# Kernel tuning notes

Hardware: AMD Instinct MI355X
Metric: run time of the kernel (lower is better)

The kernel has to match this reference:

```python
import jax, jax.numpy as jnp
import numpy as np

B, T, C = 1, 2_000_000, 16
NAN_FRAC = 0.05  # fraction of entries replaced by NaN, as the layer is a NaN-interpolation op


def setup_inputs() -> dict:
    key = jax.random.key(0)
    k_x, k_m = jax.random.split(key)
    x = jax.random.normal(k_x, (B, T, C), dtype=jnp.float32)
    nan_mask = jax.random.uniform(k_m, (B, T, C)) < NAN_FRAC
    x = jnp.where(nan_mask, jnp.float32(jnp.nan), x)
    return {"inputs": x}


def reference(inputs):
    # Vectorized form of the per-column loop: for each column, compute the
    # mean of the valid (non-NaN) entries along time and fill NaNs with it.
    # (Original code computes this per column with tf.reduce_mean + tf.map_fn
    # + tf.where/tf.fill; here it is a single fused pass.)
    mask = jnp.isnan(inputs)                       # [B, T, C]
    safe = jnp.where(mask, jnp.float32(0.0), inputs)
    valid = jnp.sum(jnp.logical_not(mask).astype(inputs.dtype), axis=1)  # [B, C]
    mean = jnp.sum(safe, axis=1) / jnp.maximum(valid, 1.0)               # [B, C]
    out = jnp.where(mask, mean[:, None, :], safe)  # broadcast NaN fill
    return out
```

## Files before the change

kernel.cpp:

```cpp
#include <hip/hip_runtime.h>

#define C_COLS 16

__global__ __launch_bounds__(256) void k_reduce(const float4* __restrict__ x4,
                                                long long n4,
                                                float* __restrict__ partials) {
    const int tid = threadIdx.x;
    const long long gid = (long long)blockIdx.x * blockDim.x + tid;
    const long long stride = (long long)gridDim.x * blockDim.x;

    float s0 = 0.f, s1 = 0.f, s2 = 0.f, s3 = 0.f;
    float c0 = 0.f, c1 = 0.f, c2 = 0.f, c3 = 0.f;

    for (long long i = gid; i < n4; i += stride) {
        float4 v = x4[i];
        bool m0 = (v.x == v.x); s0 += m0 ? v.x : 0.f; c0 += m0 ? 1.f : 0.f;
        bool m1 = (v.y == v.y); s1 += m1 ? v.y : 0.f; c1 += m1 ? 1.f : 0.f;
        bool m2 = (v.z == v.z); s2 += m2 ? v.z : 0.f; c2 += m2 ? 1.f : 0.f;
        bool m3 = (v.w == v.w); s3 += m3 ? v.w : 0.f; c3 += m3 ? 1.f : 0.f;
    }

    for (int off = 4; off < 64; off <<= 1) {
        s0 += __shfl_xor(s0, off, 64);
        s1 += __shfl_xor(s1, off, 64);
        s2 += __shfl_xor(s2, off, 64);
        s3 += __shfl_xor(s3, off, 64);
        c0 += __shfl_xor(c0, off, 64);
        c1 += __shfl_xor(c1, off, 64);
        c2 += __shfl_xor(c2, off, 64);
        c3 += __shfl_xor(c3, off, 64);
    }

    __shared__ float bsum[C_COLS];
    __shared__ float bcnt[C_COLS];
    if (tid < C_COLS) { bsum[tid] = 0.f; bcnt[tid] = 0.f; }
    __syncthreads();

    if ((tid & 63) < 4) {
        const int cb = (tid & 3) * 4;
        atomicAdd(&bsum[cb + 0], s0);
        atomicAdd(&bsum[cb + 1], s1);
        atomicAdd(&bsum[cb + 2], s2);
        atomicAdd(&bsum[cb + 3], s3);
        atomicAdd(&bcnt[cb + 0], c0);
        atomicAdd(&bcnt[cb + 1], c1);
        atomicAdd(&bcnt[cb + 2], c2);
        atomicAdd(&bcnt[cb + 3], c3);
    }
    __syncthreads();

    if (tid < C_COLS) {
        partials[(long long)blockIdx.x * 32 + tid] = bsum[tid];
        partials[(long long)blockIdx.x * 32 + 16 + tid] = bcnt[tid];
    }
}

__global__ __launch_bounds__(256) void k_final(const float* __restrict__ partials,
                                               int nb,
                                               const float* __restrict__ x,
                                               long long n4, long long n,
                                               float* __restrict__ mean_out) {
    const int tid = threadIdx.x;
    const int c = tid & 15;
    const int r0 = tid >> 4;

    float s = 0.f, cnt = 0.f;
    for (int p = r0; p < nb; p += 16) {
        s   += partials[(long long)p * 32 + c];
        cnt += partials[(long long)p * 32 + 16 + c];
    }

    __shared__ float ssum[256];
    __shared__ float scnt[256];
    ssum[tid] = s;
    scnt[tid] = cnt;
    __syncthreads();

    if (tid < 16) {
        float S = 0.f, Cn = 0.f;
        for (int r = 0; r < 16; ++r) {
            S  += ssum[r * 16 + tid];
            Cn += scnt[r * 16 + tid];
        }
        for (long long j = n4 * 4; j < n; ++j) {
            if ((int)(j % 16) == tid) {
                float v = x[j];
                if (v == v) { S += v; Cn += 1.f; }
            }
        }
        mean_out[tid] = S / fmaxf(Cn, 1.f);
    }
}

__global__ __launch_bounds__(256) void k_fill(const float4* __restrict__ x4,
                                              float4* __restrict__ o4,
                                              long long n4, long long n,
                                              const float* __restrict__ mean) {
    const int tid = threadIdx.x;
    const long long gid = (long long)blockIdx.x * blockDim.x + tid;
    const long long stride = (long long)gridDim.x * blockDim.x;

    const int cb = (int)(gid & 3) * 4;
    const float m0 = mean[cb + 0];
    const float m1 = mean[cb + 1];
    const float m2 = mean[cb + 2];
    const float m3 = mean[cb + 3];

    for (long long i = gid; i < n4; i += stride) {
        float4 v = x4[i];
        v.x = (v.x == v.x) ? v.x : m0;
        v.y = (v.y == v.y) ? v.y : m1;
        v.z = (v.z == v.z) ? v.z : m2;
        v.w = (v.w == v.w) ? v.w : m3;
        o4[i] = v;
    }

    if (blockIdx.x == 0 && tid == 0) {
        const float* x = (const float*)x4;
        float* o = (float*)o4;
        for (long long j = n4 * 4; j < n; ++j) {
            float v = x[j];
            o[j] = (v == v) ? v : mean[(int)(j % 16)];
        }
    }
}

extern "C" void kernel_launch(void* const* d_in, const int* in_sizes, int n_in,
                              void* d_out, int out_size, void* d_ws, size_t ws_size,
                              hipStream_t stream) {
    const float* x = (const float*)d_in[0];
    float* out = (float*)d_out;
    const long long n = (long long)in_sizes[0];
    const long long n4 = n / 4;

    int nb1 = 1024;
    {
        long long cap = ((long long)(ws_size / 4) - 16) / 32;
        if (cap < 1) cap = 1;
        if (nb1 > cap) nb1 = (int)cap;
    }
    float* partials = (float*)d_ws;
    float* mean = partials + (long long)nb1 * 32;

    k_reduce<<<nb1, 256, 0, stream>>>((const float4*)x, n4, partials);
    k_final<<<1, 256, 0, stream>>>(partials, nb1, x, n4, n, mean);

    const int nb3 = 2048;
    k_fill<<<nb3, 256, 0, stream>>>((const float4*)x, (float4*)out, n4, n, mean);
}
```

Baseline: 252.1 us.

## Fuse reduce, finalize and fill into one cooperative kernel with grid syncs

Replaces the three launches (reduce, single-block finalize, fill) with one cooperative kernel. Two grid-wide barriers separate the partial reduction, the block-0 mean computation and the fill pass. This removes two kernel launch gaps and may let the second read of the input hit in cache, since each thread re-reads the same float4 indices it reduced. It also adds unroll pragmas and nontemporal stores for the output. The risks are that grid.sync adds its own overhead, cooperative launch limits the grid to co-resident blocks (1024x256 with launch bounds of 4 blocks per CU), and the fill pass now uses 1024 blocks instead of 2048.

```diff
diff --git a/kernel.cpp b/kernel.cpp
--- a/kernel.cpp
+++ b/kernel.cpp
@@ -1,17 +1,26 @@
 #include <hip/hip_runtime.h>
+#include <hip/hip_cooperative_groups.h>
+
+namespace cg = cooperative_groups;
 
 #define C_COLS 16
+#define NT 256
+#define NB 1024
 
-__global__ __launch_bounds__(256) void k_reduce(const float4* __restrict__ x4,
-                                                long long n4,
-                                                float* __restrict__ partials) {
+typedef float floatx4 __attribute__((ext_vector_type(4)));
+
+__global__ __launch_bounds__(NT, 4) void k_fused(const float4* __restrict__ x4,
+                                                 float4* __restrict__ o4,
+                                                 long long n4, long long n,
+                                                 float* __restrict__ ws) {
     const int tid = threadIdx.x;
-    const long long gid = (long long)blockIdx.x * blockDim.x + tid;
-    const long long stride = (long long)gridDim.x * blockDim.x;
+    const long long gid = (long long)blockIdx.x * NT + tid;
+    const long long stride = (long long)gridDim.x * NT;
 
     float s0 = 0.f, s1 = 0.f, s2 = 0.f, s3 = 0.f;
     float c0 = 0.f, c1 = 0.f, c2 = 0.f, c3 = 0.f;
 
+    #pragma unroll 4
     for (long long i = gid; i < n4; i += stride) {
         float4 v = x4[i];
         bool m0 = (v.x == v.x); s0 += m0 ? v.x : 0.f; c0 += m0 ? 1.f : 0.f;
@@ -37,68 +46,59 @@
     __syncthreads();
 
     if ((tid & 63) < 4) {
-        const int cb = (tid & 3) * 4;
-        atomicAdd(&bsum[cb + 0], s0);
-        atomicAdd(&bsum[cb + 1], s1);
-        atomicAdd(&bsum[cb + 2], s2);
-        atomicAdd(&bsum[cb + 3], s3);
-        atomicAdd(&bcnt[cb + 0], c0);
-        atomicAdd(&bcnt[cb + 1], c1);
-        atomicAdd(&bcnt[cb + 2], c2);
-        atomicAdd(&bcnt[cb + 3], c3);
+        const int cb4 = (tid & 3) * 4;
+        atomicAdd(&bsum[cb4 + 0], s0);
+        atomicAdd(&bsum[cb4 + 1], s1);
+        atomicAdd(&bsum[cb4 + 2], s2);
+        atomicAdd(&bsum[cb4 + 3], s3);
+        atomicAdd(&bcnt[cb4 + 0], c0);
+        atomicAdd(&bcnt[cb4 + 1], c1);
+        atomicAdd(&bcnt[cb4 + 2], c2);
+        atomicAdd(&bcnt[cb4 + 3], c3);
     }
     __syncthreads();
 
     if (tid < C_COLS) {
-        partials[(long long)blockIdx.x * 32 + tid] = bsum[tid];
-        partials[(long long)blockIdx.x * 32 + 16 + tid] = bcnt[tid];
+        ws[(long long)blockIdx.x * 32 + tid] = bsum[tid];
+        ws[(long long)blockIdx.x * 32 + C_COLS + tid] = bcnt[tid];
     }
-}
+    __threadfence();
 
-__global__ __launch_bounds__(256) void k_final(const float* __restrict__ partials,
-                                               int nb,
-                                               const float* __restrict__ x,
-                                               long long n4, long long n,
-                                               float* __restrict__ mean_out) {
-    const int tid = threadIdx.x;
-    const int c = tid & 15;
-    const int r0 = tid >> 4;
+    cg::this_grid().sync();
 
-    float s = 0.f, cnt = 0.f;
-    for (int p = r0; p < nb; p += 16) {
-        s   += partials[(long long)p * 32 + c];
-        cnt += partials[(long long)p * 32 + 16 + c];
+    float* mean = ws + (long long)gridDim.x * 32;
+    if (blockIdx.x == 0) {
+        const int c = tid & 15;
+        const int r0 = tid >> 4;
+        float S = 0.f, Cn = 0.f;
+        for (int p = r0; p < (int)gridDim.x; p += 16) {
+            S  += ws[(long long)p * 32 + c];
+            Cn += ws[(long long)p * 32 + 16 + c];
+        }
+        __shared__ float ssum[NT];
+        __shared__ float scnt[NT];
+        ssum[tid] = S;
+        scnt[tid] = Cn;
+        __syncthreads();
+        if (tid < 16) {
+            float SS = 0.f, CC = 0.f;
+            for (int r = 0; r < 16; ++r) {
+                SS += ssum[r * 16 + tid];
+                CC += scnt[r * 16 + tid];
+            }
+            const float* x = (const float*)x4;
+            for (long long j = n4 * 4; j < n; ++j) {
+                if ((int)(j % 16) == tid) {
+                    float v = x[j];
+                    if (v == v) { SS += v; CC += 1.f; }
+                }
+            }
+            mean[tid] = SS / fmaxf(CC, 1.f);
+        }
+        __threadfence();
     }
 
-    __shared__ float ssum[256];
-    __shared__ float scnt[256];
-    ssum[tid] = s;
-    scnt[tid] = cnt;
-    __syncthreads();
-
-    if (tid < 16) {
-        float S = 0.f, Cn = 0.f;
-        for (int r = 0; r < 16; ++r) {
-            S  += ssum[r * 16 + tid];
-            Cn += scnt[r * 16 + tid];
-        }
-        for (long long j = n4 * 4; j < n; ++j) {
-            if ((int)(j % 16) == tid) {
-                float v = x[j];
-                if (v == v) { S += v; Cn += 1.f; }
-            }
-        }
-        mean_out[tid] = S / fmaxf(Cn, 1.f);
-    }
-}
-
-__global__ __launch_bounds__(256) void k_fill(const float4* __restrict__ x4,
-                                              float4* __restrict__ o4,
-                                              long long n4, long long n,
-                                              const float* __restrict__ mean) {
-    const int tid = threadIdx.x;
-    const long long gid = (long long)blockIdx.x * blockDim.x + tid;
-    const long long stride = (long long)gridDim.x * blockDim.x;
+    cg::this_grid().sync();
 
     const int cb = (int)(gid & 3) * 4;
     const float m0 = mean[cb + 0];
@@ -106,16 +106,19 @@
     const float m2 = mean[cb + 2];
     const float m3 = mean[cb + 3];
 
+    #pragma unroll 4
     for (long long i = gid; i < n4; i += stride) {
         float4 v = x4[i];
         v.x = (v.x == v.x) ? v.x : m0;
         v.y = (v.y == v.y) ? v.y : m1;
         v.z = (v.z == v.z) ? v.z : m2;
         v.w = (v.w == v.w) ? v.w : m3;
-        o4[i] = v;
+        floatx4 nv;
+        nv.x = v.x; nv.y = v.y; nv.z = v.z; nv.w = v.w;
+        __builtin_nontemporal_store(nv, (floatx4*)&o4[i]);
     }
 
-    if (blockIdx.x == 0 && tid == 0) {
+    if (gid == 0) {
         const float* x = (const float*)x4;
         float* o = (float*)o4;
         for (long long j = n4 * 4; j < n; ++j) {
@@ -133,18 +136,18 @@
     const long long n = (long long)in_sizes[0];
     const long long n4 = n / 4;
 
-    int nb1 = 1024;
+    int nb = NB;
     {
         long long cap = ((long long)(ws_size / 4) - 16) / 32;
         if (cap < 1) cap = 1;
-        if (nb1 > cap) nb1 = (int)cap;
+        if (nb > cap) nb = (int)cap;
     }
-    float* partials = (float*)d_ws;
-    float* mean = partials + (long long)nb1 * 32;
 
-    k_reduce<<<nb1, 256, 0, stream>>>((const float4*)x, n4, partials);
-    k_final<<<1, 256, 0, stream>>>(partials, nb1, x, n4, n, mean);
+    const float4* x4 = (const float4*)x;
+    float4* o4 = (float4*)out;
+    float* ws = (float*)d_ws;
+    long long n4v = n4, nv = n;
 
-    const int nb3 = 2048;
-    k_fill<<<nb3, 256, 0, stream>>>((const float4*)x, (float4*)out, n4, n, mean);
+    void* args[] = { (void*)&x4, (void*)&o4, (void*)&n4v, (void*)&nv, (void*)&ws };
+    (void)hipLaunchCooperativeKernel((const void*)k_fused, dim3(nb), dim3(NT), args, 0, stream);
 }
```

After: 466.7 us. 85.1% more time.
